# Optimization experiments

Hardware: AMD Instinct MI355X
Metric: run time of the kernel (lower is better)

Reference implementation:

```python
import jax, jax.numpy as jnp
import numpy as np

MASK_VALUE = -1e30


def setup_inputs() -> dict:
    key = jax.random.key(0)
    ks = jax.random.split(key, 8)
    B, N, M, D = 64, 1024, 128, 256
    c = jax.random.normal(ks[0], (B, N, D), dtype=jnp.float32)
    q = jax.random.normal(ks[1], (B, M, D), dtype=jnp.float32)
    c_mask = jax.random.randint(ks[2], (B, N), 0, 2, dtype=jnp.int32)
    q_mask = jax.random.randint(ks[3], (B, M), 0, 2, dtype=jnp.int32)
    w0 = jax.random.normal(ks[4], (D, 1), dtype=jnp.float32) * 0.06  # glorot-ish scale
    w1 = jax.random.normal(ks[5], (D, 1), dtype=jnp.float32) * 0.06
    wm = jax.random.normal(ks[6], (D,), dtype=jnp.float32) * 0.06
    bias = jnp.zeros((M,), dtype=jnp.float32)
    return {"c": c, "q": q, "c_mask": c_mask, "q_mask": q_mask,
            "w0": w0, "w1": w1, "wm": wm, "bias": bias}


def reference(c, q, c_mask, q_mask, w0, w1, wm, bias):
    # Trilinear similarity S[b,i,j] = c.w0 + q.w1 + sum_d c*wm*q + bias[j]
    sub0 = jnp.einsum('bnd,do->bno', c, w0)              # (B,N,1)
    sub1 = jnp.einsum('bmd,do->bom', q, w1)              # (B,1,M)
    sub2 = jnp.einsum('bnd,d,bmd->bnm', c, wm, q)        # (B,N,M)
    S = sub0 + sub1 + sub2 + bias                        # bias broadcast over last axis
    qm = q_mask.astype(jnp.float32)[:, None, :]          # (B,1,M)
    cm = c_mask.astype(jnp.float32)[:, :, None]          # (B,N,1)
    S_ = jax.nn.softmax(S + MASK_VALUE * (1.0 - qm), axis=-1)   # row softmax over query
    S_T = jnp.swapaxes(jax.nn.softmax(S + MASK_VALUE * (1.0 - cm), axis=1), 1, 2)  # (B,M,N)
    c2q = jnp.matmul(S_, q)                              # (B,N,D)
    q2c = jnp.matmul(jnp.matmul(S_, S_T), c)             # (B,N,D)
    return jnp.concatenate([c, c2q, c * c2q, c * q2c], axis=-1)  # (B,N,4D)
```

## Files before the change

### kernel.cpp

```cpp
#include <hip/hip_runtime.h>
#include <cfloat>

#define BB 64
#define NN 1024
#define MM 128
#define DD 256
#define MASKV (-1e30f)

__global__ __launch_bounds__(256) void k_dots(
    const float* __restrict__ c, const float* __restrict__ q,
    const int* __restrict__ qmask,
    const float* __restrict__ w0, const float* __restrict__ w1,
    const float* __restrict__ bias,
    float* __restrict__ sub0, float* __restrict__ qtermM) {
  int wave = (blockIdx.x * blockDim.x + threadIdx.x) >> 6;
  int lane = threadIdx.x & 63;
  const int total = BB * NN + BB * MM;
  if (wave >= total) return;
  const float* row;
  const float* w;
  if (wave < BB * NN) { row = c + (size_t)wave * DD; w = w0; }
  else                { row = q + (size_t)(wave - BB * NN) * DD; w = w1; }
  float4 v  = *(const float4*)(row + lane * 4);
  float4 wv = *(const float4*)(w   + lane * 4);
  float s = v.x * wv.x + v.y * wv.y + v.z * wv.z + v.w * wv.w;
  #pragma unroll
  for (int off = 32; off > 0; off >>= 1) s += __shfl_xor(s, off, 64);
  if (lane == 0) {
    if (wave < BB * NN) {
      sub0[wave] = s;
    } else {
      int r = wave - BB * NN;
      int m = r & (MM - 1);
      qtermM[r] = s + bias[m] + (qmask[r] ? 0.0f : MASKV);
    }
  }
}

__global__ __launch_bounds__(256) void k_zero(float* __restrict__ p) {
  p[blockIdx.x * 256 + threadIdx.x] = 0.0f;
}

__global__ __launch_bounds__(256) void k_score(
    const float* __restrict__ c, const float* __restrict__ q,
    const int* __restrict__ cmask, const float* __restrict__ wm,
    const float* __restrict__ sub0, const float* __restrict__ qtermM,
    float* __restrict__ S_, float* __restrict__ E,
    float* __restrict__ colsum) {
  __shared__ float cw[64 * 32];
  __shared__ float qs[128 * 36];
  __shared__ float lcs[8 * 128];
  const int b = blockIdx.y;
  const int n0 = blockIdx.x * 64;
  const int t = threadIdx.x;
  const int tx = t & 31, ty = t >> 5;

  float acc[8][4];
  #pragma unroll
  for (int i = 0; i < 8; i++)
    #pragma unroll
    for (int j = 0; j < 4; j++) acc[i][j] = 0.0f;

  float qt[4];
  #pragma unroll
  for (int j = 0; j < 4; j++) qt[j] = qtermM[b * MM + tx + j * 32];

  for (int k0 = 0; k0 < DD; k0 += 32) {
    __syncthreads();
    #pragma unroll
    for (int i = 0; i < 2; i++) {
      int idx4 = t + i * 256;
      int r = idx4 >> 3, dd = (idx4 & 7) * 4;
      float4 cv = *(const float4*)(c + (size_t)(b * NN + n0 + r) * DD + k0 + dd);
      float4 wv = *(const float4*)(wm + k0 + dd);
      cv.x *= wv.x; cv.y *= wv.y; cv.z *= wv.z; cv.w *= wv.w;
      *(float4*)(cw + r * 32 + dd) = cv;
    }
    #pragma unroll
    for (int i = 0; i < 4; i++) {
      int idx4 = t + i * 256;
      int m = idx4 >> 3, dd = (idx4 & 7) * 4;
      float4 qv = *(const float4*)(q + (size_t)(b * MM + m) * DD + k0 + dd);
      *(float4*)(qs + m * 36 + dd) = qv;
    }
    __syncthreads();
    #pragma unroll
    for (int dk = 0; dk < 32; dk += 4) {
      float4 av[8], bv[4];
      #pragma unroll
      for (int i = 0; i < 8; i++) av[i] = *(const float4*)(cw + (ty * 8 + i) * 32 + dk);
      #pragma unroll
      for (int j = 0; j < 4; j++) bv[j] = *(const float4*)(qs + (tx + j * 32) * 36 + dk);
      #pragma unroll
      for (int i = 0; i < 8; i++)
        #pragma unroll
        for (int j = 0; j < 4; j++)
          acc[i][j] += av[i].x * bv[j].x + av[i].y * bv[j].y +
                       av[i].z * bv[j].z + av[i].w * bv[j].w;
    }
  }

  float ps[4] = {0.f, 0.f, 0.f, 0.f};
  #pragma unroll
  for (int i = 0; i < 8; i++) {
    int gn = n0 + ty * 8 + i;
    float s0m = sub0[b * NN + gn] + (cmask[b * NN + gn] ? 0.0f : MASKV);
    float x[4], e[4];
    float vmax = -FLT_MAX;
    #pragma unroll
    for (int j = 0; j < 4; j++) { x[j] = acc[i][j] + qt[j]; vmax = fmaxf(vmax, x[j]); }
    #pragma unroll
    for (int off = 16; off > 0; off >>= 1) vmax = fmaxf(vmax, __shfl_xor(vmax, off, 64));
    float vsum = 0.0f;
    #pragma unroll
    for (int j = 0; j < 4; j++) { e[j] = __expf(x[j] - vmax); vsum += e[j]; }
    #pragma unroll
    for (int off = 16; off > 0; off >>= 1) vsum += __shfl_xor(vsum, off, 64);
    float inv = 1.0f / vsum;
    size_t base = (size_t)(b * NN + gn) * MM + tx;
    #pragma unroll
    for (int j = 0; j < 4; j++) {
      S_[base + j * 32] = e[j] * inv;
      float Ev = __expf(acc[i][j] + s0m);
      E[base + j * 32] = Ev;
      ps[j] += Ev;
    }
  }

  #pragma unroll
  for (int j = 0; j < 4; j++) lcs[ty * 128 + tx + j * 32] = ps[j];
  __syncthreads();
  if (t < 128) {
    float s = 0.0f;
    #pragma unroll
    for (int g = 0; g < 8; g++) s += lcs[g * 128 + t];
    atomicAdd(&colsum[b * MM + t], s);
  }
}

__global__ __launch_bounds__(256) void k_colA(
    const float* __restrict__ E, const float* __restrict__ c,
    const float* __restrict__ colsum, float* __restrict__ A) {
  __shared__ float se[32 * 64];
  __shared__ float sc[32 * 64];
  const int b = blockIdx.z;
  const int m0 = blockIdx.x * 64;
  const int d0 = blockIdx.y * 64;
  const int t = threadIdx.x;
  const int tx = t & 15;
  const int ty = t >> 4;
  const int lr = t >> 4;
  const int lc = (t & 15) * 4;

  const float* Eb = E + (size_t)b * NN * MM + m0 + lc;
  const float* cb = c + (size_t)b * NN * DD + d0 + lc;

  float4 ev0 = *(const float4*)(Eb + (size_t)lr * MM);
  float4 ev1 = *(const float4*)(Eb + (size_t)(16 + lr) * MM);
  float4 cv0 = *(const float4*)(cb + (size_t)lr * DD);
  float4 cv1 = *(const float4*)(cb + (size_t)(16 + lr) * DD);

  float acc[4][4];
  #pragma unroll
  for (int mi = 0; mi < 4; mi++)
    #pragma unroll
    for (int di = 0; di < 4; di++) acc[mi][di] = 0.0f;

  for (int n0 = 0; n0 < NN; n0 += 32) {
    *(float4*)(&se[lr * 64 + lc])        = ev0;
    *(float4*)(&se[(16 + lr) * 64 + lc]) = ev1;
    *(float4*)(&sc[lr * 64 + lc])        = cv0;
    *(float4*)(&sc[(16 + lr) * 64 + lc]) = cv1;
    __syncthreads();
    if (n0 + 32 < NN) {
      int nn = n0 + 32;
      ev0 = *(const float4*)(Eb + (size_t)(nn + lr) * MM);
      ev1 = *(const float4*)(Eb + (size_t)(nn + 16 + lr) * MM);
      cv0 = *(const float4*)(cb + (size_t)(nn + lr) * DD);
      cv1 = *(const float4*)(cb + (size_t)(nn + 16 + lr) * DD);
    }
    #pragma unroll
    for (int kk = 0; kk < 32; kk++) {
      float4 e4 = *(const float4*)(&se[kk * 64 + ty * 4]);
      float4 c4 = *(const float4*)(&sc[kk * 64 + tx * 4]);
      float em[4] = {e4.x, e4.y, e4.z, e4.w};
      float cd[4] = {c4.x, c4.y, c4.z, c4.w};
      #pragma unroll
      for (int mi = 0; mi < 4; mi++)
        #pragma unroll
        for (int di = 0; di < 4; di++) acc[mi][di] += em[mi] * cd[di];
    }
    __syncthreads();
  }

  #pragma unroll
  for (int mi = 0; mi < 4; mi++) {
    int m = m0 + ty * 4 + mi;
    float inv = 1.0f / colsum[b * MM + m];
    float4 o = make_float4(acc[mi][0] * inv, acc[mi][1] * inv,
                           acc[mi][2] * inv, acc[mi][3] * inv);
    *(float4*)(A + (size_t)(b * MM + m) * DD + d0 + tx * 4) = o;
  }
}

__global__ __launch_bounds__(256) void k_out(
    const float* __restrict__ c, const float* __restrict__ q,
    const float* __restrict__ S_, const float* __restrict__ A,
    float* __restrict__ out) {
  __shared__ float s[32 * 128];
  const int b = blockIdx.y;
  const int n0 = blockIdx.x * 32;
  const int t = threadIdx.x;
  const int dx = t & 63, ry = t >> 6;

  size_t sbase = (size_t)(b * NN + n0) * MM;
  #pragma unroll
  for (int it = 0; it < 16; it++) {
    int idx = t + it * 256;
    s[idx] = S_[sbase + idx];
  }
  __syncthreads();

  float c2q[8][4], q2c[8][4];
  #pragma unroll
  for (int i = 0; i < 8; i++)
    #pragma unroll
    for (int k = 0; k < 4; k++) { c2q[i][k] = 0.f; q2c[i][k] = 0.f; }

  for (int m = 0; m < MM; m++) {
    float4 qv = *(const float4*)(q + (size_t)(b * MM + m) * DD + dx * 4);
    float4 av = *(const float4*)(A + (size_t)(b * MM + m) * DD + dx * 4);
    #pragma unroll
    for (int i = 0; i < 8; i++) {
      float sv = s[(ry * 8 + i) * 128 + m];
      c2q[i][0] += sv * qv.x; c2q[i][1] += sv * qv.y;
      c2q[i][2] += sv * qv.z; c2q[i][3] += sv * qv.w;
      q2c[i][0] += sv * av.x; q2c[i][1] += sv * av.y;
      q2c[i][2] += sv * av.z; q2c[i][3] += sv * av.w;
    }
  }

  #pragma unroll
  for (int i = 0; i < 8; i++) {
    int gn = n0 + ry * 8 + i;
    float4 cv = *(const float4*)(c + (size_t)(b * NN + gn) * DD + dx * 4);
    size_t ob = (size_t)(b * NN + gn) * (4 * DD) + dx * 4;
    float4 o1 = make_float4(c2q[i][0], c2q[i][1], c2q[i][2], c2q[i][3]);
    float4 o2 = make_float4(cv.x * o1.x, cv.y * o1.y, cv.z * o1.z, cv.w * o1.w);
    float4 o3 = make_float4(cv.x * q2c[i][0], cv.y * q2c[i][1],
                            cv.z * q2c[i][2], cv.w * q2c[i][3]);
    *(float4*)(out + ob)            = cv;
    *(float4*)(out + ob + DD)       = o1;
    *(float4*)(out + ob + 2 * DD)   = o2;
    *(float4*)(out + ob + 3 * DD)   = o3;
  }
}

extern "C" void kernel_launch(void* const* d_in, const int* in_sizes, int n_in,
                              void* d_out, int out_size, void* d_ws, size_t ws_size,
                              hipStream_t stream) {
  const float* c     = (const float*)d_in[0];
  const float* q     = (const float*)d_in[1];
  const int*   cmask = (const int*)d_in[2];
  const int*   qmask = (const int*)d_in[3];
  const float* w0    = (const float*)d_in[4];
  const float* w1    = (const float*)d_in[5];
  const float* wm    = (const float*)d_in[6];
  const float* bias  = (const float*)d_in[7];
  float* out = (float*)d_out;
  float* ws  = (float*)d_ws;

  float* S_     = ws;
  float* E      = ws + 8388608;
  float* A      = ws + 16777216;
  float* sub0   = ws + 18874368;
  float* qtermM = ws + 18939904;
  float* colsum = ws + 18948096;

  k_dots<<<18432, 256, 0, stream>>>(c, q, qmask, w0, w1, bias, sub0, qtermM);
  k_zero<<<32, 256, 0, stream>>>(colsum);
  k_score<<<dim3(16, BB), 256, 0, stream>>>(c, q, cmask, wm, sub0, qtermM, S_, E, colsum);
  k_colA<<<dim3(2, 4, BB), 256, 0, stream>>>(E, c, colsum, A);
  k_out<<<dim3(32, BB), 256, 0, stream>>>(c, q, S_, A, out);
}
```

Measured before the change: 602.7 us.

## Compute score GEMM with split-bf16 MFMA instead of FP32 FMA

The score kernel's c*wm·q GEMM now uses bf16 MFMA 32x32x16 instructions. Each fp32 operand is split into high and low bf16 parts, and three MFMAs per step (hh, hl, lh) keep accuracy close to fp32. Tiles grow to 128 rows per block, and shared memory uses an XOR swizzle to avoid bank conflicts. The column-sum reduction moves from shared memory to wave shuffles. The cost is extra conversion work and a small loss of precision compared with exact fp32.

```diff
diff --git a/kernel.cpp b/kernel.cpp
--- a/kernel.cpp
+++ b/kernel.cpp
@@ -6,6 +6,32 @@
 #define MM 128
 #define DD 256
 #define MASKV (-1e30f)
+
+typedef __attribute__((ext_vector_type(8))) short bf16x8;
+typedef __attribute__((ext_vector_type(16))) float f32x16;
+
+__device__ __forceinline__ unsigned short f2bf(float x) {
+  union { float f; unsigned int u; } v; v.f = x;
+  unsigned int r = v.u + 0x7fffu + ((v.u >> 16) & 1u);
+  return (unsigned short)(r >> 16);
+}
+__device__ __forceinline__ float bf2f(unsigned short h) {
+  union { float f; unsigned int u; } v; v.u = ((unsigned int)h) << 16;
+  return v.f;
+}
+__device__ __forceinline__ void split8(const float* xs, uint4* hv, uint4* lv) {
+  unsigned hp[4], lp[4];
+  #pragma unroll
+  for (int p = 0; p < 4; p++) {
+    unsigned short h0 = f2bf(xs[2 * p]), h1 = f2bf(xs[2 * p + 1]);
+    unsigned short g0 = f2bf(xs[2 * p] - bf2f(h0));
+    unsigned short g1 = f2bf(xs[2 * p + 1] - bf2f(h1));
+    hp[p] = (unsigned)h0 | ((unsigned)h1 << 16);
+    lp[p] = (unsigned)g0 | ((unsigned)g1 << 16);
+  }
+  *hv = make_uint4(hp[0], hp[1], hp[2], hp[3]);
+  *lv = make_uint4(lp[0], lp[1], lp[2], lp[3]);
+}
 
 __global__ __launch_bounds__(256) void k_dots(
     const float* __restrict__ c, const float* __restrict__ q,
@@ -47,94 +73,108 @@
     const float* __restrict__ sub0, const float* __restrict__ qtermM,
     float* __restrict__ S_, float* __restrict__ E,
     float* __restrict__ colsum) {
-  __shared__ float cw[64 * 32];
-  __shared__ float qs[128 * 36];
-  __shared__ float lcs[8 * 128];
+  __shared__ unsigned short cwh[128 * 64];
+  __shared__ unsigned short cwl[128 * 64];
+  __shared__ unsigned short qhi[128 * 64];
+  __shared__ unsigned short qlo[128 * 64];
   const int b = blockIdx.y;
-  const int n0 = blockIdx.x * 64;
+  const int n0 = blockIdx.x * 128;
   const int t = threadIdx.x;
-  const int tx = t & 31, ty = t >> 5;
-
-  float acc[8][4];
-  #pragma unroll
-  for (int i = 0; i < 8; i++)
-    #pragma unroll
-    for (int j = 0; j < 4; j++) acc[i][j] = 0.0f;
+  const int w = t >> 6;
+  const int l = t & 63;
+  const int l31 = l & 31;
+  const int lh = l >> 5;
+
+  f32x16 acc[4];
+  #pragma unroll
+  for (int mb = 0; mb < 4; mb++)
+    #pragma unroll
+    for (int i = 0; i < 16; i++) acc[mb][i] = 0.0f;
+
+  for (int k0 = 0; k0 < DD; k0 += 64) {
+    __syncthreads();
+    #pragma unroll
+    for (int g = 0; g < 4; g++) {
+      int lin = t + g * 256;
+      int row = lin >> 3;
+      int kg  = (lin & 7) * 8;
+      unsigned boff = (unsigned)(row * 128 + ((kg * 2) ^ ((row & 7) << 4)));
+      float4 w0v = *(const float4*)(wm + k0 + kg);
+      float4 w1v = *(const float4*)(wm + k0 + kg + 4);
+      const float* cp = c + (size_t)(b * NN + n0 + row) * DD + k0 + kg;
+      float4 a0 = *(const float4*)cp;
+      float4 a1 = *(const float4*)(cp + 4);
+      float xs[8] = {a0.x * w0v.x, a0.y * w0v.y, a0.z * w0v.z, a0.w * w0v.w,
+                     a1.x * w1v.x, a1.y * w1v.y, a1.z * w1v.z, a1.w * w1v.w};
+      uint4 hv, lv;
+      split8(xs, &hv, &lv);
+      *(uint4*)((char*)cwh + boff) = hv;
+      *(uint4*)((char*)cwl + boff) = lv;
+      const float* qp = q + (size_t)(b * MM + row) * DD + k0 + kg;
+      float4 b0 = *(const float4*)qp;
+      float4 b1 = *(const float4*)(qp + 4);
+      float ys[8] = {b0.x, b0.y, b0.z, b0.w, b1.x, b1.y, b1.z, b1.w};
+      split8(ys, &hv, &lv);
+      *(uint4*)((char*)qhi + boff) = hv;
+      *(uint4*)((char*)qlo + boff) = lv;
+    }
+    __syncthreads();
+    #pragma unroll
+    for (int ks = 0; ks < 64; ks += 16) {
+      int ak = ks + lh * 8;
+      unsigned arow = (unsigned)(w * 32 + l31);
+      unsigned aoff = arow * 128 + (((unsigned)(ak * 2)) ^ ((arow & 7) << 4));
+      bf16x8 ah = *(const bf16x8*)((const char*)cwh + aoff);
+      bf16x8 al = *(const bf16x8*)((const char*)cwl + aoff);
+      #pragma unroll
+      for (int mb = 0; mb < 4; mb++) {
+        unsigned brow = (unsigned)(mb * 32 + l31);
+        unsigned boff2 = brow * 128 + (((unsigned)(ak * 2)) ^ ((brow & 7) << 4));
+        bf16x8 bh = *(const bf16x8*)((const char*)qhi + boff2);
+        bf16x8 bl = *(const bf16x8*)((const char*)qlo + boff2);
+        acc[mb] = __builtin_amdgcn_mfma_f32_32x32x16_bf16(ah, bh, acc[mb], 0, 0, 0);
+        acc[mb] = __builtin_amdgcn_mfma_f32_32x32x16_bf16(ah, bl, acc[mb], 0, 0, 0);
+        acc[mb] = __builtin_amdgcn_mfma_f32_32x32x16_bf16(al, bh, acc[mb], 0, 0, 0);
+      }
+    }
+  }
 
   float qt[4];
   #pragma unroll
-  for (int j = 0; j < 4; j++) qt[j] = qtermM[b * MM + tx + j * 32];
-
-  for (int k0 = 0; k0 < DD; k0 += 32) {
-    __syncthreads();
-    #pragma unroll
-    for (int i = 0; i < 2; i++) {
-      int idx4 = t + i * 256;
-      int r = idx4 >> 3, dd = (idx4 & 7) * 4;
-      float4 cv = *(const float4*)(c + (size_t)(b * NN + n0 + r) * DD + k0 + dd);
-      float4 wv = *(const float4*)(wm + k0 + dd);
-      cv.x *= wv.x; cv.y *= wv.y; cv.z *= wv.z; cv.w *= wv.w;
-      *(float4*)(cw + r * 32 + dd) = cv;
-    }
-    #pragma unroll
-    for (int i = 0; i < 4; i++) {
-      int idx4 = t + i * 256;
-      int m = idx4 >> 3, dd = (idx4 & 7) * 4;
-      float4 qv = *(const float4*)(q + (size_t)(b * MM + m) * DD + k0 + dd);
-      *(float4*)(qs + m * 36 + dd) = qv;
-    }
-    __syncthreads();
-    #pragma unroll
-    for (int dk = 0; dk < 32; dk += 4) {
-      float4 av[8], bv[4];
-      #pragma unroll
-      for (int i = 0; i < 8; i++) av[i] = *(const float4*)(cw + (ty * 8 + i) * 32 + dk);
-      #pragma unroll
-      for (int j = 0; j < 4; j++) bv[j] = *(const float4*)(qs + (tx + j * 32) * 36 + dk);
-      #pragma unroll
-      for (int i = 0; i < 8; i++)
-        #pragma unroll
-        for (int j = 0; j < 4; j++)
-          acc[i][j] += av[i].x * bv[j].x + av[i].y * bv[j].y +
-                       av[i].z * bv[j].z + av[i].w * bv[j].w;
-    }
-  }
+  for (int mb = 0; mb < 4; mb++) qt[mb] = qtermM[b * MM + mb * 32 + l31];
 
   float ps[4] = {0.f, 0.f, 0.f, 0.f};
   #pragma unroll
-  for (int i = 0; i < 8; i++) {
-    int gn = n0 + ty * 8 + i;
+  for (int r = 0; r < 16; r++) {
+    int row = (r & 3) + 8 * (r >> 2) + 4 * lh;
+    int gn = n0 + w * 32 + row;
     float s0m = sub0[b * NN + gn] + (cmask[b * NN + gn] ? 0.0f : MASKV);
-    float x[4], e[4];
+    float x[4];
     float vmax = -FLT_MAX;
     #pragma unroll
-    for (int j = 0; j < 4; j++) { x[j] = acc[i][j] + qt[j]; vmax = fmaxf(vmax, x[j]); }
+    for (int mb = 0; mb < 4; mb++) { x[mb] = acc[mb][r] + qt[mb]; vmax = fmaxf(vmax, x[mb]); }
     #pragma unroll
     for (int off = 16; off > 0; off >>= 1) vmax = fmaxf(vmax, __shfl_xor(vmax, off, 64));
+    float e[4];
     float vsum = 0.0f;
     #pragma unroll
-    for (int j = 0; j < 4; j++) { e[j] = __expf(x[j] - vmax); vsum += e[j]; }
+    for (int mb = 0; mb < 4; mb++) { e[mb] = __expf(x[mb] - vmax); vsum += e[mb]; }
     #pragma unroll
     for (int off = 16; off > 0; off >>= 1) vsum += __shfl_xor(vsum, off, 64);
     float inv = 1.0f / vsum;
-    size_t base = (size_t)(b * NN + gn) * MM + tx;
-    #pragma unroll
-    for (int j = 0; j < 4; j++) {
-      S_[base + j * 32] = e[j] * inv;
-      float Ev = __expf(acc[i][j] + s0m);
-      E[base + j * 32] = Ev;
-      ps[j] += Ev;
-    }
-  }
-
-  #pragma unroll
-  for (int j = 0; j < 4; j++) lcs[ty * 128 + tx + j * 32] = ps[j];
-  __syncthreads();
-  if (t < 128) {
-    float s = 0.0f;
-    #pragma unroll
-    for (int g = 0; g < 8; g++) s += lcs[g * 128 + t];
-    atomicAdd(&colsum[b * MM + t], s);
+    size_t base = (size_t)(b * NN + gn) * MM + l31;
+    #pragma unroll
+    for (int mb = 0; mb < 4; mb++) {
+      S_[base + mb * 32] = e[mb] * inv;
+      float Ev = __expf(acc[mb][r] + s0m);
+      E[base + mb * 32] = Ev;
+      ps[mb] += Ev;
+    }
+  }
+  #pragma unroll
+  for (int mb = 0; mb < 4; mb++) {
+    ps[mb] += __shfl_xor(ps[mb], 32, 64);
+    if (lh == 0) atomicAdd(&colsum[b * MM + mb * 32 + l31], ps[mb]);
   }
 }
 
@@ -279,7 +319,7 @@
 
   k_dots<<<18432, 256, 0, stream>>>(c, q, qmask, w0, w1, bias, sub0, qtermM);
   k_zero<<<32, 256, 0, stream>>>(colsum);
-  k_score<<<dim3(16, BB), 256, 0, stream>>>(c, q, cmask, wm, sub0, qtermM, S_, E, colsum);
+  k_score<<<dim3(8, BB), 256, 0, stream>>>(c, q, cmask, wm, sub0, qtermM, S_, E, colsum);
   k_colA<<<dim3(2, 4, BB), 256, 0, stream>>>(E, c, colsum, A);
   k_out<<<dim3(32, BB), 256, 0, stream>>>(c, q, S_, A, out);
 }
```

New measurement: 528.2 us. 12.4% less time.
